# Kernel tuning notes

Measured on AMD Instinct MI355X. Metric: run time of the kernel, lower is better.

The kernel has to match this reference:

```python
import jax, jax.numpy as jnp
import numpy as np

B, S, D = 2048, 200, 128   # batch, n_steps, embedding dim per vector
H = 64                      # hidden_dim
MASK_SCALE = 1e10


def setup_inputs() -> dict:
    key = jax.random.key(0)
    ks = jax.random.split(key, 6)
    his = jax.random.normal(ks[0], (B, S, D), dtype=jnp.float32)
    target = jax.random.normal(ks[1], (B, 1, D), dtype=jnp.float32)
    # mask == 1.0 marks padded history positions (they get -1e10 added pre-softmax)
    mask = (jax.random.uniform(ks[2], (B, S)) < 0.3).astype(jnp.float32)
    W = jax.random.normal(ks[3], (3 * D, H), dtype=jnp.float32) * 0.1
    W_bias = jnp.full((H,), 0.1, dtype=jnp.float32)
    O = jax.random.normal(ks[4], (H, 1), dtype=jnp.float32) * 0.1
    O_bias = jnp.full((1,), 0.1, dtype=jnp.float32)
    return {"his": his, "target": target, "mask": mask,
            "W": W, "W_bias": W_bias, "O": O, "O_bias": O_bias}


def reference(his, target, mask, W, W_bias, O, O_bias):
    tgt = jnp.broadcast_to(target, his.shape)          # [B,S,D] tile over steps
    diff = his - tgt
    att_vec = jnp.concatenate([his, diff, tgt], axis=2)  # [B,S,3D]
    h = jax.nn.relu(jnp.einsum('bsf,fh->bsh', att_vec, W) + W_bias)  # [B,S,H]
    alpha = jnp.einsum('bsh,ho->bso', h, O) + O_bias   # [B,S,1]
    alpha = alpha[:, :, 0] - mask * MASK_SCALE         # [B,S]
    attn = jax.nn.softmax(alpha, axis=-1)              # [B,S]
    out = jnp.einsum('bs,bsd->bd', attn, his)          # weighted-sum pooling
    return out
```

## Files before the change

kernel.cpp:

```cpp
#include <hip/hip_runtime.h>

#define B_ 2048
#define S_ 200
#define D_ 128
#define H_ 64
#define KB_ 8
#define GRID_ (B_ / KB_)
#define MASK_SCALE 1e10f

typedef __attribute__((ext_vector_type(8))) short short8_t;
typedef __attribute__((ext_vector_type(4))) float f32x4;
typedef __attribute__((ext_vector_type(4))) unsigned short ushort4_t;

__device__ __forceinline__ unsigned short f2bf(float f) {
    unsigned u = __float_as_uint(f);
    unsigned r = (u + 0x7fffu + ((u >> 16) & 1u)) >> 16;
    return (unsigned short)r;
}
__device__ __forceinline__ float bf2f(unsigned short v) {
    return __uint_as_float(((unsigned)v) << 16);
}
__device__ __forceinline__ unsigned cvt_pk_bf16(float lo, float hi) {
    unsigned r;
    asm("v_cvt_pk_bf16_f32 %0, %1, %2" : "=v"(r) : "v"(lo), "v"(hi));
    return r;
}
__device__ __forceinline__ void bar() {
    asm volatile("s_waitcnt lgkmcnt(0)\n\ts_barrier" ::: "memory");
}

__global__ __launch_bounds__(256) void prep(const float* __restrict__ W,
                                            unsigned short* __restrict__ wfrag,
                                            float* __restrict__ w23t) {
    int idx = blockIdx.x * 256 + threadIdx.x;
    int d = idx >> 6;
    int h = idx & 63;
    float w1 = W[d * H_ + h];
    float w2 = W[(D_ + d) * H_ + h];
    float w3 = W[(2 * D_ + d) * H_ + h];
    int kt = d >> 5, q = (d >> 3) & 3, j = d & 7;
    int nt = h >> 4, lm = h & 15;
    int lane = (q << 4) | lm;
    wfrag[((kt * 4 + nt) * 64 + lane) * 8 + j] = f2bf(w1 + w2);
    w23t[h * D_ + d] = w3 - w2;
}

__global__ __launch_bounds__(512, 2) void fused_kernel(const float* __restrict__ his,
                                                       const float* __restrict__ mask,
                                                       const float* __restrict__ target,
                                                       const float* __restrict__ W_bias,
                                                       const unsigned short* __restrict__ wfrag,
                                                       const float* __restrict__ w23t,
                                                       const float* __restrict__ Ovec,
                                                       float* __restrict__ out) {
    __shared__ unsigned short hisb[2][S_ * D_];
    __shared__ float alph[208];
    __shared__ float attw[208];
    __shared__ float red8[8];
    __shared__ float red8b[8];
    __shared__ float ov_s[H_];
    __shared__ float tpp[8 * H_];
    __shared__ float pool_s[7 * D_];

    const int t    = threadIdx.x;
    const int lane = t & 63;
    const int wv   = t >> 6;
    const int lm   = lane & 15;
    const int q    = lane >> 4;
    const int b0   = blockIdx.x * KB_;

    if (t < H_) ov_s[t] = Ovec[t];
    const float wb = (wv == 0) ? W_bias[lane] : 0.f;

    short8_t bfrag[16];
    #pragma unroll
    for (int f = 0; f < 16; ++f)
        bfrag[f] = *(const short8_t*)(wfrag + ((size_t)(f * 64 + lane)) * 8);
    float4 wsl[4];
    #pragma unroll
    for (int k = 0; k < 4; ++k)
        wsl[k] = *(const float4*)(w23t + lane * D_ + wv * 16 + k * 4);

    float mk;
    {
        const float4* hb4 = (const float4*)(his + (size_t)b0 * S_ * D_);
        float4 x0[13];
        #pragma unroll
        for (int j = 0; j < 13; ++j) {
            int i = t + j * 512;
            if (i < 6400) x0[j] = hb4[i];
        }
        mk = (t < S_) ? mask[(size_t)b0 * S_ + t] : 0.f;
        const float4* tg4 = (const float4*)(target + (size_t)b0 * D_) + wv * 4;
        float acc = wb;
        #pragma unroll
        for (int k = 0; k < 4; ++k) {
            float4 tv = tg4[k];
            acc = fmaf(tv.x, wsl[k].x, acc);
            acc = fmaf(tv.y, wsl[k].y, acc);
            acc = fmaf(tv.z, wsl[k].z, acc);
            acc = fmaf(tv.w, wsl[k].w, acc);
        }
        tpp[wv * 64 + lane] = acc;
        #pragma unroll
        for (int j = 0; j < 13; ++j) {
            int i = t + j * 512;
            if (i < 6400) {
                int s = i >> 5, d8 = i & 31;
                int pc = (d8 >> 1) ^ (s & 15);
                uint2 v;
                v.x = cvt_pk_bf16(x0[j].x, x0[j].y);
                v.y = cvt_pk_bf16(x0[j].z, x0[j].w);
                *(uint2*)((char*)hisb[0] + s * 256 + pc * 16 + (d8 & 1) * 8) = v;
            }
        }
    }
    __syncthreads();

    int cur = 0;
    for (int n = 0; n < KB_; ++n) {
        const int b = b0 + n;
        const bool more = (n + 1 < KB_);
        const unsigned short* hb = hisb[cur];

        float th[4];
        #pragma unroll
        for (int nt = 0; nt < 4; ++nt) {
            int h = nt * 16 + lm;
            float s0 = tpp[h] + tpp[64 + h] + tpp[128 + h] + tpp[192 + h];
            float s1 = tpp[256 + h] + tpp[320 + h] + tpp[384 + h] + tpp[448 + h];
            th[nt] = s0 + s1;
        }

        float4 x[13];
        float4 tg[4];
        float mkn = 0.f;
        if (more) {
            const float4* hb4n = (const float4*)(his + (size_t)(b + 1) * S_ * D_);
            #pragma unroll
            for (int j = 0; j < 13; ++j) {
                int i = t + j * 512;
                if (i < 6400) x[j] = hb4n[i];
            }
            const float4* tg4 = (const float4*)(target + (size_t)(b + 1) * D_) + wv * 4;
            #pragma unroll
            for (int k = 0; k < 4; ++k) tg[k] = tg4[k];
            if (t < S_) mkn = mask[(size_t)(b + 1) * S_ + t];
        }

        #pragma unroll
        for (int tt = 0; tt < 2; ++tt) {
            int tile = wv + tt * 8;
            if (tile < 13) {
                int row0 = tile * 16;
                int ar = row0 + lm; if (ar > S_ - 1) ar = S_ - 1;

                f32x4 acc[4];
                #pragma unroll
                for (int nt = 0; nt < 4; ++nt) acc[nt] = (f32x4){0.f, 0.f, 0.f, 0.f};
                #pragma unroll
                for (int kt = 0; kt < 4; ++kt) {
                    int c = (kt * 4 + q) ^ (ar & 15);
                    short8_t av = *(const short8_t*)((const char*)hb + ar * 256 + c * 16);
                    #pragma unroll
                    for (int nt = 0; nt < 4; ++nt)
                        acc[nt] = __builtin_amdgcn_mfma_f32_16x16x32_bf16(av, bfrag[kt * 4 + nt], acc[nt], 0, 0, 0);
                }
                float part[4];
                #pragma unroll
                for (int r = 0; r < 4; ++r) {
                    float sum = 0.f;
                    #pragma unroll
                    for (int nt = 0; nt < 4; ++nt) {
                        int h = nt * 16 + lm;
                        float v = acc[nt][r] + th[nt];
                        v = fmaxf(v, 0.f);
                        sum = fmaf(v, ov_s[h], sum);
                    }
                    part[r] = sum;
                }
                #pragma unroll
                for (int off = 1; off < 16; off <<= 1) {
                    #pragma unroll
                    for (int r = 0; r < 4; ++r)
                        part[r] += __shfl_xor(part[r], off);
                }
                if (lm == 0) {
                    #pragma unroll
                    for (int r = 0; r < 4; ++r)
                        alph[row0 + q * 4 + r] = part[r];
                }
            }
        }
        bar();

        float a = (t < S_) ? alph[t] - mk * MASK_SCALE : -INFINITY;
        float m = a;
        #pragma unroll
        for (int off = 1; off < 64; off <<= 1) m = fmaxf(m, __shfl_xor(m, off));
        if (lane == 0) red8[wv] = m;
        bar();
        m = red8[0];
        #pragma unroll
        for (int k = 1; k < 8; ++k) m = fmaxf(m, red8[k]);
        float e = (t < S_) ? __expf(a - m) : 0.f;
        if (t < S_) attw[t] = e;
        float ssum = e;
        #pragma unroll
        for (int off = 1; off < 64; off <<= 1) ssum += __shfl_xor(ssum, off);
        if (lane == 0) red8b[wv] = ssum;
        bar();
        float tot = red8b[0];
        #pragma unroll
        for (int k = 1; k < 8; ++k) tot += red8b[k];
        const float inv = 1.f / tot;

        const int d8 = t & 31;
        const int sg = t >> 5;
        float acc0 = 0.f, acc1 = 0.f, acc2 = 0.f, acc3 = 0.f;
        for (int s = sg; s < S_; s += 16) {
            float w = attw[s];
            int pc = (d8 >> 1) ^ (s & 15);
            ushort4_t v = *(const ushort4_t*)((const char*)hb + s * 256 + pc * 16 + (d8 & 1) * 8);
            acc0 = fmaf(w, bf2f(v[0]), acc0);
            acc1 = fmaf(w, bf2f(v[1]), acc1);
            acc2 = fmaf(w, bf2f(v[2]), acc2);
            acc3 = fmaf(w, bf2f(v[3]), acc3);
        }
        acc0 += __shfl_xor(acc0, 32);
        acc1 += __shfl_xor(acc1, 32);
        acc2 += __shfl_xor(acc2, 32);
        acc3 += __shfl_xor(acc3, 32);
        if (wv && lane < 32) {
            float4 p; p.x = acc0; p.y = acc1; p.z = acc2; p.w = acc3;
            *(float4*)(&pool_s[(wv - 1) * D_ + d8 * 4]) = p;
        }

        if (more) {
            unsigned short* hn = hisb[cur ^ 1];
            #pragma unroll
            for (int j = 0; j < 13; ++j) {
                int i = t + j * 512;
                if (i < 6400) {
                    int s = i >> 5, d8c = i & 31;
                    int pc = (d8c >> 1) ^ (s & 15);
                    uint2 v;
                    v.x = cvt_pk_bf16(x[j].x, x[j].y);
                    v.y = cvt_pk_bf16(x[j].z, x[j].w);
                    *(uint2*)((char*)hn + s * 256 + pc * 16 + (d8c & 1) * 8) = v;
                }
            }
            float acc = wb;
            #pragma unroll
            for (int k = 0; k < 4; ++k) {
                acc = fmaf(tg[k].x, wsl[k].x, acc);
                acc = fmaf(tg[k].y, wsl[k].y, acc);
                acc = fmaf(tg[k].z, wsl[k].z, acc);
                acc = fmaf(tg[k].w, wsl[k].w, acc);
            }
            tpp[wv * 64 + lane] = acc;
        }
        bar();

        if (wv == 0 && lane < 32) {
            #pragma unroll
            for (int k = 0; k < 7; ++k) {
                const float4 p = *(const float4*)(&pool_s[k * D_ + d8 * 4]);
                acc0 += p.x; acc1 += p.y; acc2 += p.z; acc3 += p.w;
            }
            float4 o;
            o.x = acc0 * inv; o.y = acc1 * inv; o.z = acc2 * inv; o.w = acc3 * inv;
            *(float4*)(out + (size_t)b * D_ + d8 * 4) = o;
        }

        mk = mkn;
        cur ^= 1;
    }
}

extern "C" void kernel_launch(void* const* d_in, const int* in_sizes, int n_in,
                              void* d_out, int out_size, void* d_ws, size_t ws_size,
                              hipStream_t stream) {
    const float* his    = (const float*)d_in[0];
    const float* target = (const float*)d_in[1];
    const float* mask   = (const float*)d_in[2];
    const float* W      = (const float*)d_in[3];
    const float* W_bias = (const float*)d_in[4];
    const float* Ovec   = (const float*)d_in[5];
    float* out = (float*)d_out;

    char* ws = (char*)d_ws;
    unsigned short* wfrag = (unsigned short*)ws;
    float* w23t           = (float*)(ws + 16384);

    prep<<<32, 256, 0, stream>>>(W, wfrag, w23t);
    fused_kernel<<<GRID_, 512, 0, stream>>>(his, mask, target, W_bias, wfrag, w23t, Ovec, out);
}
```

Before: 302.5 us.

## Fold weight preprocessing into fused kernel via LDS, drop separate prep launch

Removes the separate prep kernel launch. Each block now loads W itself, computes the combined (w1+w2) bf16 MFMA fragments and the (w3-w2) transposed weights into the unused second his buffer in shared memory, then reads its register fragments from there. It also adds scheduling barriers around the prefetch loads and unrolls the pooling loop. This trades one kernel launch and its serialization for redundant per-block weight transform work and two extra block barriers in the prologue.

```diff
diff --git a/kernel.cpp b/kernel.cpp
--- a/kernel.cpp
+++ b/kernel.cpp
@@ -29,28 +29,11 @@
     asm volatile("s_waitcnt lgkmcnt(0)\n\ts_barrier" ::: "memory");
 }
 
-__global__ __launch_bounds__(256) void prep(const float* __restrict__ W,
-                                            unsigned short* __restrict__ wfrag,
-                                            float* __restrict__ w23t) {
-    int idx = blockIdx.x * 256 + threadIdx.x;
-    int d = idx >> 6;
-    int h = idx & 63;
-    float w1 = W[d * H_ + h];
-    float w2 = W[(D_ + d) * H_ + h];
-    float w3 = W[(2 * D_ + d) * H_ + h];
-    int kt = d >> 5, q = (d >> 3) & 3, j = d & 7;
-    int nt = h >> 4, lm = h & 15;
-    int lane = (q << 4) | lm;
-    wfrag[((kt * 4 + nt) * 64 + lane) * 8 + j] = f2bf(w1 + w2);
-    w23t[h * D_ + d] = w3 - w2;
-}
-
 __global__ __launch_bounds__(512, 2) void fused_kernel(const float* __restrict__ his,
                                                        const float* __restrict__ mask,
                                                        const float* __restrict__ target,
+                                                       const float* __restrict__ W,
                                                        const float* __restrict__ W_bias,
-                                                       const unsigned short* __restrict__ wfrag,
-                                                       const float* __restrict__ w23t,
                                                        const float* __restrict__ Ovec,
                                                        float* __restrict__ out) {
     __shared__ unsigned short hisb[2][S_ * D_];
@@ -73,15 +56,9 @@
     const float wb = (wv == 0) ? W_bias[lane] : 0.f;
 
     short8_t bfrag[16];
-    #pragma unroll
-    for (int f = 0; f < 16; ++f)
-        bfrag[f] = *(const short8_t*)(wfrag + ((size_t)(f * 64 + lane)) * 8);
     float4 wsl[4];
-    #pragma unroll
-    for (int k = 0; k < 4; ++k)
-        wsl[k] = *(const float4*)(w23t + lane * D_ + wv * 16 + k * 4);
-
     float mk;
+
     {
         const float4* hb4 = (const float4*)(his + (size_t)b0 * S_ * D_);
         float4 x0[13];
@@ -90,18 +67,66 @@
             int i = t + j * 512;
             if (i < 6400) x0[j] = hb4[i];
         }
+        const float4* W4 = (const float4*)W;
+        float4 w1v[4], w2v[4], w3v[4];
+        #pragma unroll
+        for (int k = 0; k < 4; ++k) {
+            int j = t + k * 512;
+            w1v[k] = W4[j];
+            w2v[k] = W4[j + 2048];
+            w3v[k] = W4[j + 4096];
+        }
         mk = (t < S_) ? mask[(size_t)b0 * S_ + t] : 0.f;
         const float4* tg4 = (const float4*)(target + (size_t)b0 * D_) + wv * 4;
-        float acc = wb;
+        float4 tg0[4];
+        #pragma unroll
+        for (int k = 0; k < 4; ++k) tg0[k] = tg4[k];
+        __builtin_amdgcn_sched_barrier(0);
+
+        unsigned short* wf_s = hisb[1];
+        float* wdt_s = (float*)((char*)hisb[1] + 16384);
         #pragma unroll
         for (int k = 0; k < 4; ++k) {
-            float4 tv = tg4[k];
-            acc = fmaf(tv.x, wsl[k].x, acc);
-            acc = fmaf(tv.y, wsl[k].y, acc);
-            acc = fmaf(tv.z, wsl[k].z, acc);
-            acc = fmaf(tv.w, wsl[k].w, acc);
-        }
-        tpp[wv * 64 + lane] = acc;
+            int j = t + k * 512;
+            int e = 4 * j;
+            int d = e >> 6;
+            int h = e & 63;
+            float whc[4] = { w1v[k].x + w2v[k].x, w1v[k].y + w2v[k].y,
+                             w1v[k].z + w2v[k].z, w1v[k].w + w2v[k].w };
+            float wdc[4] = { w3v[k].x - w2v[k].x, w3v[k].y - w2v[k].y,
+                             w3v[k].z - w2v[k].z, w3v[k].w - w2v[k].w };
+            int kt = d >> 5, qd = (d >> 3) & 3, jj = d & 7;
+            #pragma unroll
+            for (int c = 0; c < 4; ++c) {
+                int hh = h + c;
+                int nt = hh >> 4, lmh = hh & 15;
+                int ln = (qd << 4) | lmh;
+                wf_s[((kt * 4 + nt) * 64 + ln) * 8 + jj] = f2bf(whc[c]);
+                wdt_s[hh * D_ + d] = wdc[c];
+            }
+        }
+        __syncthreads();
+
+        #pragma unroll
+        for (int f = 0; f < 16; ++f)
+            bfrag[f] = *(const short8_t*)(wf_s + (size_t)(f * 64 + lane) * 8);
+        #pragma unroll
+        for (int k = 0; k < 4; ++k)
+            wsl[k] = *(const float4*)(wdt_s + lane * D_ + wv * 16 + k * 4);
+
+        {
+            float acc = wb;
+            #pragma unroll
+            for (int k = 0; k < 4; ++k) {
+                acc = fmaf(tg0[k].x, wsl[k].x, acc);
+                acc = fmaf(tg0[k].y, wsl[k].y, acc);
+                acc = fmaf(tg0[k].z, wsl[k].z, acc);
+                acc = fmaf(tg0[k].w, wsl[k].w, acc);
+            }
+            tpp[wv * 64 + lane] = acc;
+        }
+        __syncthreads();
+
         #pragma unroll
         for (int j = 0; j < 13; ++j) {
             int i = t + j * 512;
@@ -147,6 +172,7 @@
             for (int k = 0; k < 4; ++k) tg[k] = tg4[k];
             if (t < S_) mkn = mask[(size_t)(b + 1) * S_ + t];
         }
+        __builtin_amdgcn_sched_barrier(0);
 
         #pragma unroll
         for (int tt = 0; tt < 2; ++tt) {
@@ -218,6 +244,7 @@
         const int d8 = t & 31;
         const int sg = t >> 5;
         float acc0 = 0.f, acc1 = 0.f, acc2 = 0.f, acc3 = 0.f;
+        #pragma unroll 4
         for (int s = sg; s < S_; s += 16) {
             float w = attw[s];
             int pc = (d8 >> 1) ^ (s & 15);
@@ -289,10 +316,5 @@
     const float* Ovec   = (const float*)d_in[5];
     float* out = (float*)d_out;
 
-    char* ws = (char*)d_ws;
-    unsigned short* wfrag = (unsigned short*)ws;
-    float* w23t           = (float*)(ws + 16384);
-
-    prep<<<32, 256, 0, stream>>>(W, wfrag, w23t);
-    fused_kernel<<<GRID_, 512, 0, stream>>>(his, mask, target, W_bias, wfrag, w23t, Ovec, out);
-}
+    fused_kernel<<<GRID_, 512, 0, stream>>>(his, mask, target, W, W_bias, Ovec, out);
+}
```

Measured after the change: 302.7 us. No clear change (+0.1%).
